# Optimization experiments

Hardware: AMD Instinct MI355X
Metric: run time of the kernel (lower is better)

## Reference

```python
import jax, jax.numpy as jnp
import numpy as np


def setup_inputs() -> dict:
    key = jax.random.key(0)
    k1, k2 = jax.random.split(key)
    X = jax.random.normal(k1, (8192, 10000), dtype=jnp.float32)
    # logits parameter, xavier_normal init: std = sqrt(2/(fan_in+fan_out))
    std = np.sqrt(2.0 / (256 + 10000)).astype(np.float32)
    logits = jax.random.normal(k2, (256, 10000), dtype=jnp.float32) * std
    return {"X": X, "logits": logits, "temp": 1}


def reference(X, logits, temp):
    # Gumbel-softmax with hard=True (straight-through), matching F.gumbel_softmax.
    gkey = jax.random.key(42)
    g = jax.random.gumbel(gkey, logits.shape, dtype=logits.dtype)
    y_soft = jax.nn.softmax((logits + g) / temp, axis=-1)          # [S, D]
    idx = jnp.argmax(y_soft, axis=-1)                               # [S]
    y_hard = jax.nn.one_hot(idx, logits.shape[-1], dtype=y_soft.dtype)
    # hard forward, soft backward: y_hard - sg(y_soft) + y_soft
    selections = y_hard - jax.lax.stop_gradient(y_soft) + y_soft    # [S, D]
    # Y = X @ selections^T  (one-hot rows -> column gather of X)
    Y = jnp.matmul(X, selections.T)                                 # [B, S]
    return Y
```

## Files before the change

### kernel.cpp

```cpp
#include <hip/hip_runtime.h>
#include <stdint.h>


#define S_ROWS 256
#define D_COLS 10000
#define B_ROWS 8192

__device__ __forceinline__ void threefry2x32(uint32_t& x0, uint32_t& x1) {
  const uint32_t k0 = 0u;
  const uint32_t k1 = 42u;
  const uint32_t k2 = 0x1BD11BDAu ^ k0 ^ k1;
  x0 += k0; x1 += k1;
#define TFR(r) { x0 += x1; x1 = (x1 << (r)) | (x1 >> (32 - (r))); x1 ^= x0; }
  TFR(13) TFR(15) TFR(26) TFR(6)   x0 += k1; x1 += k2 + 1u;
  TFR(17) TFR(29) TFR(16) TFR(24)  x0 += k2; x1 += k0 + 2u;
  TFR(13) TFR(15) TFR(26) TFR(6)   x0 += k0; x1 += k1 + 3u;
  TFR(17) TFR(29) TFR(16) TFR(24)  x0 += k1; x1 += k2 + 4u;
  TFR(13) TFR(15) TFR(26) TFR(6)   x0 += k2; x1 += k0 + 5u;
#undef TFR
}

__device__ __forceinline__ uint32_t jax_random_bits(uint32_t i) {
  uint32_t x0 = 0u, x1 = i;
  threefry2x32(x0, x1);
  return x0 ^ x1;
}

__device__ __forceinline__ float uniform_from_bits(uint32_t bits) {
  uint32_t fb = (bits >> 9) | 0x3f800000u;
  float u = __uint_as_float(fb) - 1.0f;
  if (u <= 0.0f) u = 1.17549435e-38f;
  return u;
}

__device__ __forceinline__ float gumbel_f(uint32_t bits) {
  float u  = uniform_from_bits(bits);
  float nl = -logf(u);
  return -logf(nl);
}

__device__ __forceinline__ double gumbel_d(uint32_t bits) {
  float u = uniform_from_bits(bits);
  double lu = log((double)u);
  return -log(-lu);
}

#define ARGMAX_THREADS 1024
#define CAND_MAX 64

__global__ __launch_bounds__(ARGMAX_THREADS)
void argmax_gumbel_kernel(const float* __restrict__ logits, int* __restrict__ idx_out) {
  const int s   = blockIdx.x;
  const int tid = threadIdx.x;
  const int base = s * D_COLS;

  __shared__ float zbuf[D_COLS];
  __shared__ float sv[ARGMAX_THREADS];
  __shared__ int   si[ARGMAX_THREADS];
  __shared__ int   n_cand;
  __shared__ int   cand[CAND_MAX];

  if (tid == 0) n_cand = 0;

  float best = -1.0e30f;
  int   bi   = 0;
  for (int d = tid; d < D_COLS; d += ARGMAX_THREADS) {
    uint32_t bits = jax_random_bits((uint32_t)(base + d));
    float z = logits[base + d] + gumbel_f(bits);
    zbuf[d] = z;
    if (z > best) { best = z; bi = d; }
  }
  sv[tid] = best; si[tid] = bi;
  __syncthreads();
  for (int off = ARGMAX_THREADS / 2; off > 0; off >>= 1) {
    if (tid < off) {
      float ov = sv[tid + off]; int oi = si[tid + off];
      if (ov > sv[tid] || (ov == sv[tid] && oi < si[tid])) { sv[tid] = ov; si[tid] = oi; }
    }
    __syncthreads();
  }

  const float thresh = sv[0] - 1.0e-3f;
  for (int d = tid; d < D_COLS; d += ARGMAX_THREADS) {
    if (zbuf[d] >= thresh) {
      int pos = atomicAdd(&n_cand, 1);
      if (pos < CAND_MAX) cand[pos] = d;
    }
  }
  __syncthreads();

  if (tid == 0) {
    int    nc   = n_cand < CAND_MAX ? n_cand : CAND_MAX;
    double bz   = -1.0e300;
    int    bidx = 0x7fffffff;
    for (int i = 0; i < nc; ++i) {
      int d = cand[i];
      double z = (double)logits[base + d] + gumbel_d(jax_random_bits((uint32_t)(base + d)));
      if (z > bz || (z == bz && d < bidx)) { bz = z; bidx = d; }
    }
    idx_out[s] = bidx;
  }
}

#define ROWS_PER_BLOCK 8
__global__ __launch_bounds__(256)
void gather_cols_kernel(const float* __restrict__ X,
                        const int* __restrict__ idx,
                        float* __restrict__ Y) {
  const int s   = threadIdx.x;
  const int col = idx[s];
  const long b0 = (long)blockIdx.x * ROWS_PER_BLOCK;
  float v[ROWS_PER_BLOCK];
#pragma unroll
  for (int r = 0; r < ROWS_PER_BLOCK; ++r)
    v[r] = X[(b0 + r) * D_COLS + col];
#pragma unroll
  for (int r = 0; r < ROWS_PER_BLOCK; ++r)
    Y[(b0 + r) * S_ROWS + s] = v[r];
}

extern "C" void kernel_launch(void* const* d_in, const int* in_sizes, int n_in,
                              void* d_out, int out_size, void* d_ws, size_t ws_size,
                              hipStream_t stream) {
  const float* X      = (const float*)d_in[0];
  const float* logits = (const float*)d_in[1];
  float*       Y      = (float*)d_out;
  int*         idx    = (int*)d_ws;

  argmax_gumbel_kernel<<<S_ROWS, ARGMAX_THREADS, 0, stream>>>(logits, idx);
  gather_cols_kernel<<<B_ROWS / ROWS_PER_BLOCK, 256, 0, stream>>>(X, idx, Y);
}
```

Baseline: 416.5 us.

## Stream full X rows coalesced and scatter selected columns via LDS linked lists

Replaces the per-output strided column gather with a kernel that streams each X row with coalesced float4 loads. Selected columns are matched through a shared-memory column-to-selection linked list built from the argmax indices. Outputs are staged in LDS and written back contiguously. This trades reading all of X for fully coalesced, high-occupancy memory traffic in place of scattered single-float loads. It also adds per-block setup of a 40KB head table.

```diff
diff --git a/kernel.cpp b/kernel.cpp
--- a/kernel.cpp
+++ b/kernel.cpp
@@ -102,21 +102,62 @@
   }
 }
 
-#define ROWS_PER_BLOCK 8
-__global__ __launch_bounds__(256)
-void gather_cols_kernel(const float* __restrict__ X,
-                        const int* __restrict__ idx,
-                        float* __restrict__ Y) {
-  const int s   = threadIdx.x;
-  const int col = idx[s];
-  const long b0 = (long)blockIdx.x * ROWS_PER_BLOCK;
-  float v[ROWS_PER_BLOCK];
-#pragma unroll
-  for (int r = 0; r < ROWS_PER_BLOCK; ++r)
-    v[r] = X[(b0 + r) * D_COLS + col];
-#pragma unroll
-  for (int r = 0; r < ROWS_PER_BLOCK; ++r)
-    Y[(b0 + r) * S_ROWS + s] = v[r];
+#define GATHER_THREADS 512
+#define GATHER_ROWS 8
+#define ROW_F4 (D_COLS / 4)
+
+__global__ __launch_bounds__(GATHER_THREADS)
+void stream_gather_kernel(const float* __restrict__ X,
+                          const int* __restrict__ idx,
+                          float* __restrict__ Y) {
+  __shared__ int   head[D_COLS];
+  __shared__ int   nxt[S_ROWS];
+  __shared__ float yrow[GATHER_ROWS * S_ROWS];
+  const int tid = threadIdx.x;
+
+  for (int i = tid; i < D_COLS; i += GATHER_THREADS) head[i] = -1;
+  __syncthreads();
+  if (tid < S_ROWS) {
+    int c = idx[tid];
+    nxt[tid] = atomicExch(&head[c], tid);
+  }
+  __syncthreads();
+
+  const int wave = tid >> 6;
+  const int lane = tid & 63;
+  const long b   = (long)blockIdx.x * GATHER_ROWS + wave;
+  const float4* __restrict__ xrow  = (const float4*)(X + b * D_COLS);
+  const int4*   __restrict__ head4 = (const int4*)head;
+  float* yw = &yrow[wave * S_ROWS];
+
+#define PROC(vv, hh)                                                  \
+  {                                                                   \
+    if ((hh).x >= 0) { int s=(hh).x; do { yw[s]=(vv).x; s=nxt[s]; } while (s>=0); } \
+    if ((hh).y >= 0) { int s=(hh).y; do { yw[s]=(vv).y; s=nxt[s]; } while (s>=0); } \
+    if ((hh).z >= 0) { int s=(hh).z; do { yw[s]=(vv).z; s=nxt[s]; } while (s>=0); } \
+    if ((hh).w >= 0) { int s=(hh).w; do { yw[s]=(vv).w; s=nxt[s]; } while (s>=0); } \
+  }
+
+  int i = lane;
+  for (; i + 64 < ROW_F4; i += 128) {
+    float4 v0 = xrow[i];
+    float4 v1 = xrow[i + 64];
+    int4   h0 = head4[i];
+    int4   h1 = head4[i + 64];
+    PROC(v0, h0)
+    PROC(v1, h1)
+  }
+  for (; i < ROW_F4; i += 64) {
+    float4 v = xrow[i];
+    int4   h = head4[i];
+    PROC(v, h)
+  }
+#undef PROC
+
+  __syncthreads();
+  const long o0 = (long)blockIdx.x * GATHER_ROWS * S_ROWS;
+  for (int k = tid; k < GATHER_ROWS * S_ROWS; k += GATHER_THREADS)
+    Y[o0 + k] = yrow[k];
 }
 
 extern "C" void kernel_launch(void* const* d_in, const int* in_sizes, int n_in,
@@ -128,5 +169,5 @@
   int*         idx    = (int*)d_ws;
 
   argmax_gumbel_kernel<<<S_ROWS, ARGMAX_THREADS, 0, stream>>>(logits, idx);
-  gather_cols_kernel<<<B_ROWS / ROWS_PER_BLOCK, 256, 0, stream>>>(X, idx, Y);
+  stream_gather_kernel<<<B_ROWS / GATHER_ROWS, GATHER_THREADS, 0, stream>>>(X, idx, Y);
 }
```

Measured after the change: 456.9 us. 9.7% more time.
